# Performance work log

Measured on AMD Instinct MI355X. Metric: run time of the kernel, lower is better.

The kernel has to match this reference:

```python
import jax, jax.numpy as jnp
import numpy as np

EPS = 1e-9


def _resolve(circle_pos, circle_radius, aabb_pos, aabb_half):
    Nc = circle_pos.shape[0]
    Na = aabb_pos.shape[0]

    # ---- circle vs circle: push apart along center-to-center normal ----
    d = circle_pos[:, None, :] - circle_pos[None, :, :]          # [Nc,Nc,2]
    d2 = jnp.sum(d * d, axis=-1)                                 # [Nc,Nc]
    off_diag = ~jnp.eye(Nc, dtype=bool)
    dist = jnp.sqrt(jnp.where(d2 > EPS, d2, 1.0))
    pen = circle_radius[:, None] + circle_radius[None, :] - dist
    hit = off_diag & (d2 > EPS) & (pen > 0)
    normal = d / dist[..., None]
    # each body moves half the penetration toward itself; summing over the
    # full (symmetric) matrix resolves every unordered pair exactly once
    corr_cc = jnp.sum(jnp.where(hit[..., None], 0.5 * pen[..., None] * normal, 0.0), axis=1)

    # ---- aabb vs aabb: push along minimum-overlap axis ----
    da = aabb_pos[:, None, :] - aabb_pos[None, :, :]             # [Na,Na,2]
    ov = aabb_half[:, None, :] + aabb_half[None, :, :] - jnp.abs(da)
    hit_a = (~jnp.eye(Na, dtype=bool)) & (ov[..., 0] > 0) & (ov[..., 1] > 0)
    sgn = jnp.where(da >= 0, 1.0, -1.0)
    use_x = ov[..., 0] <= ov[..., 1]
    zeros = jnp.zeros_like(ov[..., 0])
    push_x = jnp.stack([0.5 * ov[..., 0] * sgn[..., 0], zeros], axis=-1)
    push_y = jnp.stack([zeros, 0.5 * ov[..., 1] * sgn[..., 1]], axis=-1)
    push = jnp.where(use_x[..., None], push_x, push_y)
    corr_aa = jnp.sum(jnp.where(hit_a[..., None], push, 0.0), axis=1)

    # ---- circle vs aabb: closest point on box ----
    rel = circle_pos[:, None, :] - aabb_pos[None, :, :]          # [Nc,Na,2]
    closest = jnp.clip(rel, -aabb_half[None, :, :], aabb_half[None, :, :])
    diff = rel - closest
    dd2 = jnp.sum(diff * diff, axis=-1)
    ddist = jnp.sqrt(jnp.where(dd2 > EPS, dd2, 1.0))
    pen_ca = circle_radius[:, None] - ddist
    hit_ca = (dd2 > EPS) & (pen_ca > 0)
    n_ca = diff / ddist[..., None]
    push_ca = jnp.where(hit_ca[..., None], 0.5 * pen_ca[..., None] * n_ca, 0.0)
    corr_c = jnp.sum(push_ca, axis=1)     # on circles
    corr_a = -jnp.sum(push_ca, axis=0)    # equal-and-opposite on boxes

    new_circle = circle_pos + corr_cc + corr_c
    new_aabb = aabb_pos + corr_aa + corr_a
    return jnp.concatenate([new_circle, new_aabb], axis=0)   # [Nc+Na, 2]


def setup_inputs() -> dict:
    key = jax.random.key(0)
    k1, k2, k3, k4 = jax.random.split(key, 4)
    circle_pos = jax.random.normal(k1, (4096, 2), dtype=jnp.float32)
    circle_radius = jax.random.uniform(k2, (4096,), dtype=jnp.float32)
    aabb_pos = jax.random.normal(k3, (2048, 2), dtype=jnp.float32)
    aabb_half = jax.random.uniform(k4, (2048, 2), dtype=jnp.float32)
    return {"circle_pos": circle_pos, "circle_radius": circle_radius,
            "aabb_pos": aabb_pos, "aabb_half": aabb_half}


def reference(circle_pos, circle_radius, aabb_pos, aabb_half):
    return _resolve(circle_pos, circle_radius, aabb_pos, aabb_half)
```

## Files before the change

kernel.cpp:

```cpp
#include <hip/hip_runtime.h>
#include <math.h>

#define EPS 1e-9f

__device__ __forceinline__ int tri_off(int I) { return I * (193 - I) / 2; }

__global__ __launch_bounds__(256)
void collide_ws(const float2* __restrict__ cpos,
                const float*  __restrict__ crad,
                const float2* __restrict__ apos,
                const float2* __restrict__ ahalf,
                float2* __restrict__ ws,
                int Nc) {
    const int lane = threadIdx.x & 63;
    const int w    = threadIdx.x >> 6;
    const int t    = blockIdx.x * 4 + w;

    int I = (int)((193.0f - sqrtf((float)(37249 - 8 * t))) * 0.5f);
    while (tri_off(I + 1) <= t) ++I;
    while (tri_off(I) > t) --I;
    const int J = I + (t - tri_off(I));

    const int tileC  = Nc >> 6;
    const bool bodyC = I < tileC;
    const bool partC = J < tileC;

    __shared__ float4 Jd[4][128];

    {
        const int j = (J << 6) + lane;
        float4 q;
        if (partC) {
            const float2 c = cpos[j];
            q = make_float4(c.x, c.y, 0.5f * crad[j], 0.0f);
        } else {
            const float2 a = apos[j - Nc];
            const float2 h = ahalf[j - Nc];
            q = make_float4(a.x, a.y, h.x, h.y);
        }
        Jd[w][lane]      = q;
        Jd[w][lane + 64] = q;
    }
    __syncthreads();

    const int i = (I << 6) + lane;
    float4 me;
    if (bodyC) {
        const float2 c = cpos[i];
        me = make_float4(c.x, c.y, 0.5f * crad[i], 0.0f);
    } else {
        const float2 a = apos[i - Nc];
        const float2 h = ahalf[i - Nc];
        me = make_float4(a.x, a.y, h.x, h.y);
    }

    float ax = 0.0f, ay = 0.0f;
    const int src = (lane + 1) & 63;

    if (I != J) {
        float gx = 0.0f, gy = 0.0f;
        if (partC) {
            const float px = me.x, py = me.y, rih = me.z;
            #pragma unroll 4
            for (int m = 0; m < 64; ++m) {
                const float4 q = Jd[w][lane + m];
                const float dx = q.x - px, dy = q.y - py;
                const float d2 = fmaf(dx, dx, dy * dy);
                const float r  = __builtin_amdgcn_rsqf(d2);
                const float s  = fmaxf(fmaf(rih + q.z, r, -0.5f), 0.0f);
                const float fx = s * dx, fy = s * dy;
                ax -= fx; ay -= fy;
                gx += fx; gy += fy;
                gx = __shfl(gx, src, 64);
                gy = __shfl(gy, src, 64);
            }
        } else if (bodyC) {
            const float px = me.x, py = me.y, rih = me.z;
            #pragma unroll 4
            for (int m = 0; m < 64; ++m) {
                const float4 q = Jd[w][lane + m];
                const float rx = q.x - px, ry = q.y - py;
                const float cx = fminf(fmaxf(rx, -q.z), q.z);
                const float cy = fminf(fmaxf(ry, -q.w), q.w);
                const float dx = rx - cx, dy = ry - cy;
                const float d2 = fmaf(dx, dx, dy * dy);
                const float r  = __builtin_amdgcn_rsqf(d2);
                float s = fmaxf(fmaf(rih, r, -0.5f), 0.0f);
                s = (d2 > EPS) ? s : 0.0f;
                const float fx = s * dx, fy = s * dy;
                ax -= fx; ay -= fy;
                gx += fx; gy += fy;
                gx = __shfl(gx, src, 64);
                gy = __shfl(gy, src, 64);
            }
        } else {
            const float bx = me.x, by = me.y, hx = me.z, hy = me.w;
            #pragma unroll 4
            for (int m = 0; m < 64; ++m) {
                const float4 q = Jd[w][lane + m];
                const float dqx = q.x - bx, dqy = q.y - by;
                const float ovx = (hx + q.z) - fabsf(dqx);
                const float ovy = (hy + q.w) - fabsf(dqy);
                const bool hit = fminf(ovx, ovy) > 0.0f;
                const bool ux  = ovx <= ovy;
                const float fx = (hit && ux)  ? copysignf(0.5f * ovx, dqx) : 0.0f;
                const float fy = (hit && !ux) ? copysignf(0.5f * ovy, dqy) : 0.0f;
                ax -= fx; ay -= fy;
                gx += fx; gy += fy;
                gx = __shfl(gx, src, 64);
                gy = __shfl(gy, src, 64);
            }
        }
        ws[(J * 96 + I) * 64 + lane] = make_float2(gx, gy);
    } else {
        if (bodyC) {
            const float px = me.x, py = me.y, rih = me.z;
            #pragma unroll 7
            for (int k = 1; k < 64; ++k) {
                const float4 q = Jd[w][lane + k];
                const float dx = px - q.x, dy = py - q.y;
                const float d2 = fmaf(dx, dx, dy * dy);
                const float r  = __builtin_amdgcn_rsqf(d2);
                const float s  = fmaxf(fmaf(rih + q.z, r, -0.5f), 0.0f);
                ax = fmaf(s, dx, ax); ay = fmaf(s, dy, ay);
            }
        } else {
            const float bx = me.x, by = me.y, hx = me.z, hy = me.w;
            #pragma unroll 7
            for (int k = 1; k < 64; ++k) {
                const float4 q = Jd[w][lane + k];
                const float dax = bx - q.x, day = by - q.y;
                const float ovx = (hx + q.z) - fabsf(dax);
                const float ovy = (hy + q.w) - fabsf(day);
                const bool hit = fminf(ovx, ovy) > 0.0f;
                const bool ux  = ovx <= ovy;
                ax += (hit && ux)  ? copysignf(0.5f * ovx, dax) : 0.0f;
                ay += (hit && !ux) ? copysignf(0.5f * ovy, day) : 0.0f;
            }
        }
        ax += me.x; ay += me.y;
    }

    ws[(I * 96 + J) * 64 + lane] = make_float2(ax, ay);
}

__global__ __launch_bounds__(64)
void reduce_ws(const float2* __restrict__ ws, float2* __restrict__ out) {
    const int T = blockIdx.x;
    const int l = threadIdx.x;
    const float2* row = ws + (size_t)(T * 96) * 64 + l;
    float sx = 0.0f, sy = 0.0f;
    #pragma unroll 8
    for (int P = 0; P < 96; ++P) {
        const float2 v = row[(size_t)P * 64];
        sx += v.x; sy += v.y;
    }
    out[(T << 6) + l] = make_float2(sx, sy);
}

__global__ __launch_bounds__(256)
void collide_atomic(const float2* __restrict__ cpos,
                    const float*  __restrict__ crad,
                    const float2* __restrict__ apos,
                    const float2* __restrict__ ahalf,
                    float* __restrict__ out,
                    int Nc) {
    const int lane = threadIdx.x & 63;
    const int w    = threadIdx.x >> 6;
    const int t    = blockIdx.x * 4 + w;

    int I = (int)((193.0f - sqrtf((float)(37249 - 8 * t))) * 0.5f);
    while (tri_off(I + 1) <= t) ++I;
    while (tri_off(I) > t) --I;
    const int J = I + (t - tri_off(I));

    const int tileC  = Nc >> 6;
    const bool bodyC = I < tileC;
    const bool partC = J < tileC;

    __shared__ float4 Jd[4][128];

    {
        const int j = (J << 6) + lane;
        float4 q;
        if (partC) {
            const float2 c = cpos[j];
            q = make_float4(c.x, c.y, 0.5f * crad[j], 0.0f);
        } else {
            const float2 a = apos[j - Nc];
            const float2 h = ahalf[j - Nc];
            q = make_float4(a.x, a.y, h.x, h.y);
        }
        Jd[w][lane]      = q;
        Jd[w][lane + 64] = q;
    }
    __syncthreads();

    const int i = (I << 6) + lane;
    float4 me;
    if (bodyC) {
        const float2 c = cpos[i];
        me = make_float4(c.x, c.y, 0.5f * crad[i], 0.0f);
    } else {
        const float2 a = apos[i - Nc];
        const float2 h = ahalf[i - Nc];
        me = make_float4(a.x, a.y, h.x, h.y);
    }

    float ax = 0.0f, ay = 0.0f;
    const int src = (lane + 1) & 63;

    if (I != J) {
        float gx = 0.0f, gy = 0.0f;
        if (partC) {
            const float px = me.x, py = me.y, rih = me.z;
            #pragma unroll 4
            for (int m = 0; m < 64; ++m) {
                const float4 q = Jd[w][lane + m];
                const float dx = q.x - px, dy = q.y - py;
                const float d2 = fmaf(dx, dx, dy * dy);
                const float r  = __builtin_amdgcn_rsqf(d2);
                const float s  = fmaxf(fmaf(rih + q.z, r, -0.5f), 0.0f);
                const float fx = s * dx, fy = s * dy;
                ax -= fx; ay -= fy;
                gx += fx; gy += fy;
                gx = __shfl(gx, src, 64);
                gy = __shfl(gy, src, 64);
            }
        } else if (bodyC) {
            const float px = me.x, py = me.y, rih = me.z;
            #pragma unroll 4
            for (int m = 0; m < 64; ++m) {
                const float4 q = Jd[w][lane + m];
                const float rx = q.x - px, ry = q.y - py;
                const float cx = fminf(fmaxf(rx, -q.z), q.z);
                const float cy = fminf(fmaxf(ry, -q.w), q.w);
                const float dx = rx - cx, dy = ry - cy;
                const float d2 = fmaf(dx, dx, dy * dy);
                const float r  = __builtin_amdgcn_rsqf(d2);
                float s = fmaxf(fmaf(rih, r, -0.5f), 0.0f);
                s = (d2 > EPS) ? s : 0.0f;
                const float fx = s * dx, fy = s * dy;
                ax -= fx; ay -= fy;
                gx += fx; gy += fy;
                gx = __shfl(gx, src, 64);
                gy = __shfl(gy, src, 64);
            }
        } else {
            const float bx = me.x, by = me.y, hx = me.z, hy = me.w;
            #pragma unroll 4
            for (int m = 0; m < 64; ++m) {
                const float4 q = Jd[w][lane + m];
                const float dqx = q.x - bx, dqy = q.y - by;
                const float ovx = (hx + q.z) - fabsf(dqx);
                const float ovy = (hy + q.w) - fabsf(dqy);
                const bool hit = fminf(ovx, ovy) > 0.0f;
                const bool ux  = ovx <= ovy;
                const float fx = (hit && ux)  ? copysignf(0.5f * ovx, dqx) : 0.0f;
                const float fy = (hit && !ux) ? copysignf(0.5f * ovy, dqy) : 0.0f;
                ax -= fx; ay -= fy;
                gx += fx; gy += fy;
                gx = __shfl(gx, src, 64);
                gy = __shfl(gy, src, 64);
            }
        }
        atomicAdd(&out[(((J << 6) + lane) << 1)],     gx);
        atomicAdd(&out[(((J << 6) + lane) << 1) + 1], gy);
    } else {
        if (bodyC) {
            const float px = me.x, py = me.y, rih = me.z;
            #pragma unroll 7
            for (int k = 1; k < 64; ++k) {
                const float4 q = Jd[w][lane + k];
                const float dx = px - q.x, dy = py - q.y;
                const float d2 = fmaf(dx, dx, dy * dy);
                const float r  = __builtin_amdgcn_rsqf(d2);
                const float s  = fmaxf(fmaf(rih + q.z, r, -0.5f), 0.0f);
                ax = fmaf(s, dx, ax); ay = fmaf(s, dy, ay);
            }
        } else {
            const float bx = me.x, by = me.y, hx = me.z, hy = me.w;
            #pragma unroll 7
            for (int k = 1; k < 64; ++k) {
                const float4 q = Jd[w][lane + k];
                const float dax = bx - q.x, day = by - q.y;
                const float ovx = (hx + q.z) - fabsf(dax);
                const float ovy = (hy + q.w) - fabsf(day);
                const bool hit = fminf(ovx, ovy) > 0.0f;
                const bool ux  = ovx <= ovy;
                ax += (hit && ux)  ? copysignf(0.5f * ovx, dax) : 0.0f;
                ay += (hit && !ux) ? copysignf(0.5f * ovy, day) : 0.0f;
            }
        }
        ax += me.x; ay += me.y;
    }

    atomicAdd(&out[(i << 1)],     ax);
    atomicAdd(&out[(i << 1) + 1], ay);
}

extern "C" void kernel_launch(void* const* d_in, const int* in_sizes, int n_in,
                              void* d_out, int out_size, void* d_ws, size_t ws_size,
                              hipStream_t stream) {
    (void)n_in;

    const float2* cpos  = (const float2*)d_in[0];
    const float*  crad  = (const float*) d_in[1];
    const float2* apos  = (const float2*)d_in[2];
    const float2* ahalf = (const float2*)d_in[3];

    const int Nc = in_sizes[1];

    const int tile_pairs = (96 * 97) / 2;
    const int blocks = tile_pairs / 4;

    const size_t ws_need = (size_t)96 * 96 * 64 * sizeof(float2);

    if (d_ws != nullptr && ws_size >= ws_need) {
        float2* ws = (float2*)d_ws;
        collide_ws<<<blocks, 256, 0, stream>>>(cpos, crad, apos, ahalf, ws, Nc);
        reduce_ws<<<96, 64, 0, stream>>>(ws, (float2*)d_out);
    } else {
        hipMemsetAsync(d_out, 0, (size_t)out_size * sizeof(float), stream);
        collide_atomic<<<blocks, 256, 0, stream>>>(cpos, crad, apos, ahalf,
                                                   (float*)d_out, Nc);
    }
}
```

Measured before the change: 78.22 us.

## Replace symmetric triangular tile pairing with full gather over all tile pairs

The workspace path now launches one wave per ordered tile pair (96x96) instead of per unordered pair, so each body accumulates only its own force and needs no shuffle ring or counter-force writeback. Pair interactions are computed twice, but the loop body loses the per-iteration cross-lane shuffles and uses a broadcast LDS read instead of a per-lane offset read. The triangular index decode is also dropped in favour of a simple divide. The atomic fallback path is unchanged apart from where the block count is computed.

Measured after the change: 79.74 us. No clear change (+1.9%).

```diff
diff --git a/kernel.cpp b/kernel.cpp
--- a/kernel.cpp
+++ b/kernel.cpp
@@ -3,15 +3,165 @@
 
 #define EPS 1e-9f
 
+__global__ __launch_bounds__(256)
+void collide_gather(const float2* __restrict__ cpos,
+                    const float*  __restrict__ crad,
+                    const float2* __restrict__ apos,
+                    const float2* __restrict__ ahalf,
+                    float2* __restrict__ ws,
+                    int Nc) {
+    const int lane = threadIdx.x & 63;
+    const int w    = threadIdx.x >> 6;
+    const int t    = blockIdx.x * 4 + w;
+    const int I    = t / 96;
+    const int J    = t - I * 96;
+
+    const int tileC = Nc >> 6;
+    const bool IC = I < tileC;
+    const bool JC = J < tileC;
+
+    __shared__ float4 Jd[4][128];
+
+    {
+        const int j = (J << 6) + lane;
+        float4 q;
+        if (JC) {
+            const float2 c = cpos[j];
+            q = make_float4(c.x, c.y, 0.5f * crad[j], 0.0f);
+        } else {
+            const float2 a = apos[j - Nc];
+            const float2 h = ahalf[j - Nc];
+            q = make_float4(a.x, a.y, h.x, h.y);
+        }
+        Jd[w][lane]      = q;
+        Jd[w][lane + 64] = q;
+    }
+    __syncthreads();
+
+    const int i = (I << 6) + lane;
+    float4 me;
+    if (IC) {
+        const float2 c = cpos[i];
+        me = make_float4(c.x, c.y, 0.5f * crad[i], 0.0f);
+    } else {
+        const float2 a = apos[i - Nc];
+        const float2 h = ahalf[i - Nc];
+        me = make_float4(a.x, a.y, h.x, h.y);
+    }
+
+    float ax = 0.0f, ay = 0.0f;
+
+    if (I != J) {
+        if (IC && JC) {
+            const float px = me.x, py = me.y, rih = me.z;
+            #pragma unroll 8
+            for (int m = 0; m < 64; ++m) {
+                const float4 q = Jd[w][m];
+                const float dx = px - q.x, dy = py - q.y;
+                const float d2 = fmaf(dx, dx, dy * dy);
+                const float r  = __builtin_amdgcn_rsqf(d2);
+                const float s  = fmaxf(fmaf(rih + q.z, r, -0.5f), 0.0f);
+                ax = fmaf(s, dx, ax); ay = fmaf(s, dy, ay);
+            }
+        } else if (IC) {
+            const float px = me.x, py = me.y, rih = me.z;
+            #pragma unroll 8
+            for (int m = 0; m < 64; ++m) {
+                const float4 q = Jd[w][m];
+                const float relx = px - q.x, rely = py - q.y;
+                const float cx = fminf(fmaxf(relx, -q.z), q.z);
+                const float cy = fminf(fmaxf(rely, -q.w), q.w);
+                const float dx = relx - cx, dy = rely - cy;
+                const float d2 = fmaf(dx, dx, dy * dy);
+                const float r  = __builtin_amdgcn_rsqf(d2);
+                float s = fmaxf(fmaf(rih, r, -0.5f), 0.0f);
+                s = (d2 > EPS) ? s : 0.0f;
+                ax = fmaf(s, dx, ax); ay = fmaf(s, dy, ay);
+            }
+        } else if (JC) {
+            const float bx = me.x, by = me.y, hx = me.z, hy = me.w;
+            #pragma unroll 8
+            for (int m = 0; m < 64; ++m) {
+                const float4 q = Jd[w][m];
+                const float relx = q.x - bx, rely = q.y - by;
+                const float cx = fminf(fmaxf(relx, -hx), hx);
+                const float cy = fminf(fmaxf(rely, -hy), hy);
+                const float dx = relx - cx, dy = rely - cy;
+                const float d2 = fmaf(dx, dx, dy * dy);
+                const float r  = __builtin_amdgcn_rsqf(d2);
+                float s = fmaxf(fmaf(q.z, r, -0.5f), 0.0f);
+                s = (d2 > EPS) ? s : 0.0f;
+                ax = fmaf(-s, dx, ax); ay = fmaf(-s, dy, ay);
+            }
+        } else {
+            const float bx = me.x, by = me.y, hx = me.z, hy = me.w;
+            #pragma unroll 8
+            for (int m = 0; m < 64; ++m) {
+                const float4 q = Jd[w][m];
+                const float dax = bx - q.x, day = by - q.y;
+                const float ovx = (hx + q.z) - fabsf(dax);
+                const float ovy = (hy + q.w) - fabsf(day);
+                const bool hit = fminf(ovx, ovy) > 0.0f;
+                const bool ux  = ovx <= ovy;
+                ax += (hit && ux)  ? copysignf(0.5f * ovx, dax) : 0.0f;
+                ay += (hit && !ux) ? copysignf(0.5f * ovy, day) : 0.0f;
+            }
+        }
+    } else {
+        if (IC) {
+            const float px = me.x, py = me.y, rih = me.z;
+            #pragma unroll 7
+            for (int k = 1; k < 64; ++k) {
+                const float4 q = Jd[w][lane + k];
+                const float dx = px - q.x, dy = py - q.y;
+                const float d2 = fmaf(dx, dx, dy * dy);
+                const float r  = __builtin_amdgcn_rsqf(d2);
+                const float s  = fmaxf(fmaf(rih + q.z, r, -0.5f), 0.0f);
+                ax = fmaf(s, dx, ax); ay = fmaf(s, dy, ay);
+            }
+        } else {
+            const float bx = me.x, by = me.y, hx = me.z, hy = me.w;
+            #pragma unroll 7
+            for (int k = 1; k < 64; ++k) {
+                const float4 q = Jd[w][lane + k];
+                const float dax = bx - q.x, day = by - q.y;
+                const float ovx = (hx + q.z) - fabsf(dax);
+                const float ovy = (hy + q.w) - fabsf(day);
+                const bool hit = fminf(ovx, ovy) > 0.0f;
+                const bool ux  = ovx <= ovy;
+                ax += (hit && ux)  ? copysignf(0.5f * ovx, dax) : 0.0f;
+                ay += (hit && !ux) ? copysignf(0.5f * ovy, day) : 0.0f;
+            }
+        }
+        ax += me.x; ay += me.y;
+    }
+
+    ws[(I * 96 + J) * 64 + lane] = make_float2(ax, ay);
+}
+
+__global__ __launch_bounds__(64)
+void reduce_ws(const float2* __restrict__ ws, float2* __restrict__ out) {
+    const int T = blockIdx.x;
+    const int l = threadIdx.x;
+    const float2* row = ws + (size_t)(T * 96) * 64 + l;
+    float sx = 0.0f, sy = 0.0f;
+    #pragma unroll 8
+    for (int P = 0; P < 96; ++P) {
+        const float2 v = row[(size_t)P * 64];
+        sx += v.x; sy += v.y;
+    }
+    out[(T << 6) + l] = make_float2(sx, sy);
+}
+
 __device__ __forceinline__ int tri_off(int I) { return I * (193 - I) / 2; }
 
 __global__ __launch_bounds__(256)
-void collide_ws(const float2* __restrict__ cpos,
-                const float*  __restrict__ crad,
-                const float2* __restrict__ apos,
-                const float2* __restrict__ ahalf,
-                float2* __restrict__ ws,
-                int Nc) {
+void collide_atomic(const float2* __restrict__ cpos,
+                    const float*  __restrict__ crad,
+                    const float2* __restrict__ apos,
+                    const float2* __restrict__ ahalf,
+                    float* __restrict__ out,
+                    int Nc) {
     const int lane = threadIdx.x & 63;
     const int w    = threadIdx.x >> 6;
     const int t    = blockIdx.x * 4 + w;
@@ -111,7 +261,8 @@
                 gy = __shfl(gy, src, 64);
             }
         }
-        ws[(J * 96 + I) * 64 + lane] = make_float2(gx, gy);
+        atomicAdd(&out[(((J << 6) + lane) << 1)],     gx);
+        atomicAdd(&out[(((J << 6) + lane) << 1) + 1], gy);
     } else {
         if (bodyC) {
             const float px = me.x, py = me.y, rih = me.z;
@@ -141,160 +292,6 @@
         ax += me.x; ay += me.y;
     }
 
-    ws[(I * 96 + J) * 64 + lane] = make_float2(ax, ay);
-}
-
-__global__ __launch_bounds__(64)
-void reduce_ws(const float2* __restrict__ ws, float2* __restrict__ out) {
-    const int T = blockIdx.x;
-    const int l = threadIdx.x;
-    const float2* row = ws + (size_t)(T * 96) * 64 + l;
-    float sx = 0.0f, sy = 0.0f;
-    #pragma unroll 8
-    for (int P = 0; P < 96; ++P) {
-        const float2 v = row[(size_t)P * 64];
-        sx += v.x; sy += v.y;
-    }
-    out[(T << 6) + l] = make_float2(sx, sy);
-}
-
-__global__ __launch_bounds__(256)
-void collide_atomic(const float2* __restrict__ cpos,
-                    const float*  __restrict__ crad,
-                    const float2* __restrict__ apos,
-                    const float2* __restrict__ ahalf,
-                    float* __restrict__ out,
-                    int Nc) {
-    const int lane = threadIdx.x & 63;
-    const int w    = threadIdx.x >> 6;
-    const int t    = blockIdx.x * 4 + w;
-
-    int I = (int)((193.0f - sqrtf((float)(37249 - 8 * t))) * 0.5f);
-    while (tri_off(I + 1) <= t) ++I;
-    while (tri_off(I) > t) --I;
-    const int J = I + (t - tri_off(I));
-
-    const int tileC  = Nc >> 6;
-    const bool bodyC = I < tileC;
-    const bool partC = J < tileC;
-
-    __shared__ float4 Jd[4][128];
-
-    {
-        const int j = (J << 6) + lane;
-        float4 q;
-        if (partC) {
-            const float2 c = cpos[j];
-            q = make_float4(c.x, c.y, 0.5f * crad[j], 0.0f);
-        } else {
-            const float2 a = apos[j - Nc];
-            const float2 h = ahalf[j - Nc];
-            q = make_float4(a.x, a.y, h.x, h.y);
-        }
-        Jd[w][lane]      = q;
-        Jd[w][lane + 64] = q;
-    }
-    __syncthreads();
-
-    const int i = (I << 6) + lane;
-    float4 me;
-    if (bodyC) {
-        const float2 c = cpos[i];
-        me = make_float4(c.x, c.y, 0.5f * crad[i], 0.0f);
-    } else {
-        const float2 a = apos[i - Nc];
-        const float2 h = ahalf[i - Nc];
-        me = make_float4(a.x, a.y, h.x, h.y);
-    }
-
-    float ax = 0.0f, ay = 0.0f;
-    const int src = (lane + 1) & 63;
-
-    if (I != J) {
-        float gx = 0.0f, gy = 0.0f;
-        if (partC) {
-            const float px = me.x, py = me.y, rih = me.z;
-            #pragma unroll 4
-            for (int m = 0; m < 64; ++m) {
-                const float4 q = Jd[w][lane + m];
-                const float dx = q.x - px, dy = q.y - py;
-                const float d2 = fmaf(dx, dx, dy * dy);
-                const float r  = __builtin_amdgcn_rsqf(d2);
-                const float s  = fmaxf(fmaf(rih + q.z, r, -0.5f), 0.0f);
-                const float fx = s * dx, fy = s * dy;
-                ax -= fx; ay -= fy;
-                gx += fx; gy += fy;
-                gx = __shfl(gx, src, 64);
-                gy = __shfl(gy, src, 64);
-            }
-        } else if (bodyC) {
-            const float px = me.x, py = me.y, rih = me.z;
-            #pragma unroll 4
-            for (int m = 0; m < 64; ++m) {
-                const float4 q = Jd[w][lane + m];
-                const float rx = q.x - px, ry = q.y - py;
-                const float cx = fminf(fmaxf(rx, -q.z), q.z);
-                const float cy = fminf(fmaxf(ry, -q.w), q.w);
-                const float dx = rx - cx, dy = ry - cy;
-                const float d2 = fmaf(dx, dx, dy * dy);
-                const float r  = __builtin_amdgcn_rsqf(d2);
-                float s = fmaxf(fmaf(rih, r, -0.5f), 0.0f);
-                s = (d2 > EPS) ? s : 0.0f;
-                const float fx = s * dx, fy = s * dy;
-                ax -= fx; ay -= fy;
-                gx += fx; gy += fy;
-                gx = __shfl(gx, src, 64);
-                gy = __shfl(gy, src, 64);
-            }
-        } else {
-            const float bx = me.x, by = me.y, hx = me.z, hy = me.w;
-            #pragma unroll 4
-            for (int m = 0; m < 64; ++m) {
-                const float4 q = Jd[w][lane + m];
-                const float dqx = q.x - bx, dqy = q.y - by;
-                const float ovx = (hx + q.z) - fabsf(dqx);
-                const float ovy = (hy + q.w) - fabsf(dqy);
-                const bool hit = fminf(ovx, ovy) > 0.0f;
-                const bool ux  = ovx <= ovy;
-                const float fx = (hit && ux)  ? copysignf(0.5f * ovx, dqx) : 0.0f;
-                const float fy = (hit && !ux) ? copysignf(0.5f * ovy, dqy) : 0.0f;
-                ax -= fx; ay -= fy;
-                gx += fx; gy += fy;
-                gx = __shfl(gx, src, 64);
-                gy = __shfl(gy, src, 64);
-            }
-        }
-        atomicAdd(&out[(((J << 6) + lane) << 1)],     gx);
-        atomicAdd(&out[(((J << 6) + lane) << 1) + 1], gy);
-    } else {
-        if (bodyC) {
-            const float px = me.x, py = me.y, rih = me.z;
-            #pragma unroll 7
-            for (int k = 1; k < 64; ++k) {
-                const float4 q = Jd[w][lane + k];
-                const float dx = px - q.x, dy = py - q.y;
-                const float d2 = fmaf(dx, dx, dy * dy);
-                const float r  = __builtin_amdgcn_rsqf(d2);
-                const float s  = fmaxf(fmaf(rih + q.z, r, -0.5f), 0.0f);
-                ax = fmaf(s, dx, ax); ay = fmaf(s, dy, ay);
-            }
-        } else {
-            const float bx = me.x, by = me.y, hx = me.z, hy = me.w;
-            #pragma unroll 7
-            for (int k = 1; k < 64; ++k) {
-                const float4 q = Jd[w][lane + k];
-                const float dax = bx - q.x, day = by - q.y;
-                const float ovx = (hx + q.z) - fabsf(dax);
-                const float ovy = (hy + q.w) - fabsf(day);
-                const bool hit = fminf(ovx, ovy) > 0.0f;
-                const bool ux  = ovx <= ovy;
-                ax += (hit && ux)  ? copysignf(0.5f * ovx, dax) : 0.0f;
-                ay += (hit && !ux) ? copysignf(0.5f * ovy, day) : 0.0f;
-            }
-        }
-        ax += me.x; ay += me.y;
-    }
-
     atomicAdd(&out[(i << 1)],     ax);
     atomicAdd(&out[(i << 1) + 1], ay);
 }
@@ -311,17 +308,16 @@
 
     const int Nc = in_sizes[1];
 
-    const int tile_pairs = (96 * 97) / 2;
-    const int blocks = tile_pairs / 4;
-
     const size_t ws_need = (size_t)96 * 96 * 64 * sizeof(float2);
 
     if (d_ws != nullptr && ws_size >= ws_need) {
+        const int blocks = (96 * 96) / 4;
         float2* ws = (float2*)d_ws;
-        collide_ws<<<blocks, 256, 0, stream>>>(cpos, crad, apos, ahalf, ws, Nc);
+        collide_gather<<<blocks, 256, 0, stream>>>(cpos, crad, apos, ahalf, ws, Nc);
         reduce_ws<<<96, 64, 0, stream>>>(ws, (float2*)d_out);
     } else {
         hipMemsetAsync(d_out, 0, (size_t)out_size * sizeof(float), stream);
+        const int blocks = ((96 * 97) / 2) / 4;
         collide_atomic<<<blocks, 256, 0, stream>>>(cpos, crad, apos, ahalf,
                                                    (float*)d_out, Nc);
     }
```
